# Kernel optimization log

Measured on AMD Instinct MI355X. Metric: run time of the kernel, lower is better.

## Reference

```python
import jax, jax.numpy as jnp
import numpy as np

PATCH_SIZE = 15

def setup_inputs() -> dict:
    key = jax.random.key(0)
    input_image = jax.random.normal(key, (32, 3, 512, 512), dtype=jnp.float32)
    return {"input_image": input_image}

def reference(input_image) -> jnp.ndarray:
    p = PATCH_SIZE // 2
    # reflect-pad H and W only (NCHW), matching F.pad(..., (p,p,p,p), mode='reflect')
    padded = jnp.pad(input_image, ((0, 0), (0, 0), (p, p), (p, p)), mode='reflect')
    dark_channel = jnp.min(padded, axis=1)        # [B, H+2p, W+2p]
    dark_channel_min = jnp.min(dark_channel, axis=1)  # [B, W+2p]
    dark_channel_prior = jnp.min(dark_channel_min, axis=1)  # [B]
    return jnp.mean(dark_channel_prior)
```

## Files before the change

### kernel.cpp

```cpp
#include <hip/hip_runtime.h>
#include <math.h>


#define ELEMS_PER_BATCH 786432
#define VEC4_PER_BATCH  196608
#define BLOCKS_PER_BATCH 64
#define VEC4_PER_BLOCK  (VEC4_PER_BATCH / BLOCKS_PER_BATCH)
#define THREADS 256
#define VEC4_PER_THREAD (VEC4_PER_BLOCK / THREADS)

__global__ __launch_bounds__(THREADS) void dcp_batch_min_partial(
        const float* __restrict__ in, float* __restrict__ partial) {
    const int b  = blockIdx.y;
    const int bx = blockIdx.x;
    const int t  = threadIdx.x;

    const float4* base = reinterpret_cast<const float4*>(in) +
                         (size_t)b * VEC4_PER_BATCH + (size_t)bx * VEC4_PER_BLOCK;

    float m = INFINITY;
#pragma unroll
    for (int i = 0; i < VEC4_PER_THREAD; ++i) {
        float4 v = base[i * THREADS + t];
        m = fminf(m, fminf(fminf(v.x, v.y), fminf(v.z, v.w)));
    }

#pragma unroll
    for (int off = 32; off > 0; off >>= 1)
        m = fminf(m, __shfl_down(m, off, 64));

    __shared__ float smem[THREADS / 64];
    if ((t & 63) == 0) smem[t >> 6] = m;
    __syncthreads();
    if (t == 0) {
        float r = smem[0];
#pragma unroll
        for (int w = 1; w < THREADS / 64; ++w) r = fminf(r, smem[w]);
        partial[b * BLOCKS_PER_BATCH + bx] = r;
    }
}

__global__ __launch_bounds__(64) void dcp_finalize(
        const float* __restrict__ partial, float* __restrict__ out) {
    const int t = threadIdx.x;
    float v = 0.0f;
    if (t < 32) {
        float m = INFINITY;
#pragma unroll 8
        for (int i = 0; i < BLOCKS_PER_BATCH; ++i)
            m = fminf(m, partial[t * BLOCKS_PER_BATCH + i]);
        v = m;
    }
#pragma unroll
    for (int off = 32; off > 0; off >>= 1)
        v += __shfl_down(v, off, 64);
    if (t == 0) out[0] = v * (1.0f / 32.0f);
}

extern "C" void kernel_launch(void* const* d_in, const int* in_sizes, int n_in,
                              void* d_out, int out_size, void* d_ws, size_t ws_size,
                              hipStream_t stream) {
    const float* in = (const float*)d_in[0];
    float* out = (float*)d_out;
    float* partial = (float*)d_ws;

    dim3 grid(BLOCKS_PER_BATCH, 32);
    dcp_batch_min_partial<<<grid, THREADS, 0, stream>>>(in, partial);
    dcp_finalize<<<1, 64, 0, stream>>>(partial, out);
}
```

Before: 146.0 us.

## Fuse finalize into reduction kernel via last-block atomic counter, add nontemporal loads

Merges the two-kernel reduction into one kernel in which the last block to finish, detected through an atomic counter, reduces the per-block partial minima and writes the mean. The input loads become nontemporal. This removes the second kernel launch and its dependency gap but adds a memset launch, threadfences and an atomic per block.

```diff
diff --git a/kernel.cpp b/kernel.cpp
--- a/kernel.cpp
+++ b/kernel.cpp
@@ -2,26 +2,29 @@
 #include <math.h>
 
 
-#define ELEMS_PER_BATCH 786432
 #define VEC4_PER_BATCH  196608
 #define BLOCKS_PER_BATCH 64
 #define VEC4_PER_BLOCK  (VEC4_PER_BATCH / BLOCKS_PER_BATCH)
 #define THREADS 256
 #define VEC4_PER_THREAD (VEC4_PER_BLOCK / THREADS)
+#define NBLOCKS (BLOCKS_PER_BATCH * 32)
 
-__global__ __launch_bounds__(THREADS) void dcp_batch_min_partial(
-        const float* __restrict__ in, float* __restrict__ partial) {
+typedef float f4 __attribute__((ext_vector_type(4)));
+
+__global__ __launch_bounds__(THREADS) void dcp_fused(
+        const float* __restrict__ in, float* __restrict__ out,
+        unsigned int* __restrict__ counter, float* __restrict__ partial) {
     const int b  = blockIdx.y;
     const int bx = blockIdx.x;
     const int t  = threadIdx.x;
 
-    const float4* base = reinterpret_cast<const float4*>(in) +
-                         (size_t)b * VEC4_PER_BATCH + (size_t)bx * VEC4_PER_BLOCK;
+    const f4* base = reinterpret_cast<const f4*>(in) +
+                     (size_t)b * VEC4_PER_BATCH + (size_t)bx * VEC4_PER_BLOCK;
 
     float m = INFINITY;
 #pragma unroll
     for (int i = 0; i < VEC4_PER_THREAD; ++i) {
-        float4 v = base[i * THREADS + t];
+        f4 v = __builtin_nontemporal_load(base + i * THREADS + t);
         m = fminf(m, fminf(fminf(v.x, v.y), fminf(v.z, v.w)));
     }
 
@@ -30,31 +33,40 @@
         m = fminf(m, __shfl_down(m, off, 64));
 
     __shared__ float smem[THREADS / 64];
+    __shared__ bool last;
     if ((t & 63) == 0) smem[t >> 6] = m;
     __syncthreads();
     if (t == 0) {
-        float r = smem[0];
+        float r = fminf(fminf(smem[0], smem[1]), fminf(smem[2], smem[3]));
+        partial[b * BLOCKS_PER_BATCH + bx] = r;
+        __threadfence();
+        unsigned int prev = atomicAdd(counter, 1u);
+        last = (prev == NBLOCKS - 1);
+    }
+    __syncthreads();
+    if (!last) return;
+
+    __threadfence();
+    const int batch = t >> 3;
+    const int sub   = t & 7;
+    float r = INFINITY;
 #pragma unroll
-        for (int w = 1; w < THREADS / 64; ++w) r = fminf(r, smem[w]);
-        partial[b * BLOCKS_PER_BATCH + bx] = r;
+    for (int i = 0; i < 8; ++i)
+        r = fminf(r, partial[batch * BLOCKS_PER_BATCH + sub * 8 + i]);
+#pragma unroll
+    for (int off = 1; off < 8; off <<= 1)
+        r = fminf(r, __shfl_xor(r, off, 64));
+
+    __shared__ float bmin[32];
+    if (sub == 0) bmin[batch] = r;
+    __syncthreads();
+    if (t < 64) {
+        float v = (t < 32) ? bmin[t] : 0.0f;
+#pragma unroll
+        for (int off = 32; off > 0; off >>= 1)
+            v += __shfl_down(v, off, 64);
+        if (t == 0) out[0] = v * (1.0f / 32.0f);
     }
-}
-
-__global__ __launch_bounds__(64) void dcp_finalize(
-        const float* __restrict__ partial, float* __restrict__ out) {
-    const int t = threadIdx.x;
-    float v = 0.0f;
-    if (t < 32) {
-        float m = INFINITY;
-#pragma unroll 8
-        for (int i = 0; i < BLOCKS_PER_BATCH; ++i)
-            m = fminf(m, partial[t * BLOCKS_PER_BATCH + i]);
-        v = m;
-    }
-#pragma unroll
-    for (int off = 32; off > 0; off >>= 1)
-        v += __shfl_down(v, off, 64);
-    if (t == 0) out[0] = v * (1.0f / 32.0f);
 }
 
 extern "C" void kernel_launch(void* const* d_in, const int* in_sizes, int n_in,
@@ -62,9 +74,10 @@
                               hipStream_t stream) {
     const float* in = (const float*)d_in[0];
     float* out = (float*)d_out;
-    float* partial = (float*)d_ws;
+    unsigned int* counter = (unsigned int*)d_ws;
+    float* partial = (float*)((char*)d_ws + 256);
 
+    hipMemsetAsync(counter, 0, sizeof(unsigned int), stream);
     dim3 grid(BLOCKS_PER_BATCH, 32);
-    dcp_batch_min_partial<<<grid, THREADS, 0, stream>>>(in, partial);
-    dcp_finalize<<<1, 64, 0, stream>>>(partial, out);
+    dcp_fused<<<grid, THREADS, 0, stream>>>(in, out, counter, partial);
 }
```

Measured after the change: 232.0 us. 1.59x slower.
